# Kernel tuning notes

Hardware: AMD Instinct MI355X
Metric: run time of the kernel (lower is better)

## Reference

```python
import jax, jax.numpy as jnp
import numpy as np

NUM_NODES = 512
NUM_EDGES = 512
EMB_DIM = 128
HIDDEN = 256
NUM_INC = 8192


def setup_inputs() -> dict:
    key = jax.random.key(0)
    ks = jax.random.split(key, 8)
    X = jax.random.normal(ks[0], (NUM_NODES, EMB_DIM), dtype=jnp.float32)
    V = jax.random.randint(ks[1], (NUM_INC,), 0, NUM_NODES, dtype=jnp.int64)
    E = jax.random.randint(ks[2], (NUM_INC,), 0, NUM_EDGES, dtype=jnp.int64)
    # MLP params, torch nn.Linear layout: W (out, in), y = x @ W.T + b
    lim1 = 1.0 / np.sqrt(2 * EMB_DIM)
    W1 = jax.random.uniform(ks[3], (HIDDEN, 2 * EMB_DIM), minval=-lim1, maxval=lim1, dtype=jnp.float32)
    b1 = jax.random.uniform(ks[4], (HIDDEN,), minval=-lim1, maxval=lim1, dtype=jnp.float32)
    lim2 = 1.0 / np.sqrt(HIDDEN)
    W2 = jax.random.uniform(ks[5], (1, HIDDEN), minval=-lim2, maxval=lim2, dtype=jnp.float32)
    b2 = jax.random.uniform(ks[6], (1,), minval=-lim2, maxval=lim2, dtype=jnp.float32)
    return {"X": X, "V": V, "E": E, "W1": W1, "b1": b1, "W2": W2, "b2": b2}


def reference(X, V, E, W1, b1, W2, b2):
    d = X.shape[-1]
    # scatter-mean of gathered node embeddings into edges; empty edges -> 0 (nan_to_num)
    sums = jax.ops.segment_sum(X[V], E, num_segments=NUM_EDGES)          # (M, d)
    cnt = jax.ops.segment_sum(jnp.ones((V.shape[0],), X.dtype), E, num_segments=NUM_EDGES)
    eX = jnp.where(cnt[:, None] > 0, sums / jnp.maximum(cnt[:, None], 1.0), 0.0)
    # cat([X_expanded, eX_expanded]) @ W1.T == X @ W1[:, :d].T + eX @ W1[:, d:].T (broadcast add)
    hX = X @ W1[:, :d].T                                                 # (N, H)
    hE = eX @ W1[:, d:].T                                                # (M, H)
    hidden = jax.nn.relu(hX[:, None, :] + hE[None, :, :] + b1)           # (N, M, H)
    logits = jnp.einsum('nmh,h->nm', hidden, W2[0]) + b2[0]              # (N, M)
    prob = jax.nn.sigmoid(logits)
    prob = jnp.nan_to_num(prob, nan=0.5)
    prob = jnp.clip(prob, 1e-6, 1.0 - 1e-6)
    return prob
```

## Files before the change

### kernel.cpp

```cpp
#include <hip/hip_runtime.h>
#include <math.h>

#define NN 512
#define MM 512
#define DD 128
#define HH 256

typedef float     v4f __attribute__((ext_vector_type(4)));
typedef _Float16  h8  __attribute__((ext_vector_type(8)));
typedef _Float16  h2  __attribute__((ext_vector_type(2)));


__global__ __launch_bounds__(256) void k_stage(
    const float* __restrict__ X, const int* __restrict__ V,
    const int* __restrict__ E, const float* __restrict__ W1,
    const float* __restrict__ b1, _Float16* __restrict__ A,
    _Float16* __restrict__ C, int ninc)
{
    __shared__ int   lst[8192];
    __shared__ float eXp[2 * DD];
    __shared__ float eXs[DD];
    __shared__ int   cnt_s;

    const int b = blockIdx.x;
    const int t = threadIdx.x;

    if (b < MM) {
        if (t == 0) cnt_s = 0;
        __syncthreads();
        const int nq = ninc >> 2;
        for (int c = t; c < nq; c += 256) {
            int4 e4 = ((const int4*)E)[c];
            int base = c * 4;
            if (e4.x == b) lst[atomicAdd(&cnt_s, 1)] = V[base + 0];
            if (e4.y == b) lst[atomicAdd(&cnt_s, 1)] = V[base + 1];
            if (e4.z == b) lst[atomicAdd(&cnt_s, 1)] = V[base + 2];
            if (e4.w == b) lst[atomicAdd(&cnt_s, 1)] = V[base + 3];
        }
        __syncthreads();
        const int cnt = cnt_s;

        const int d = t & 127, half = t >> 7;
        float a0 = 0.f, a1 = 0.f;
        int j = half;
        for (; j + 2 < cnt; j += 4) {
            int v0 = lst[j], v1 = lst[j + 2];
            a0 += X[v0 * DD + d];
            a1 += X[v1 * DD + d];
        }
        for (; j < cnt; j += 2) a0 += X[lst[j] * DD + d];
        eXp[half * DD + d] = a0 + a1;
        __syncthreads();
        if (t < DD) {
            float inv = cnt > 0 ? 1.0f / (float)cnt : 0.0f;
            eXs[t] = (eXp[t] + eXp[DD + t]) * inv;
        }
        __syncthreads();

        const float* w = W1 + t * (2 * DD) + DD;
        v4f dv = (v4f)(0.f);
        #pragma unroll 8
        for (int k = 0; k < DD; k += 4)
            dv += (*(const v4f*)(w + k)) * (*(const v4f*)(eXs + k));
        C[b * HH + t] = (_Float16)(b1[t] + dv.x + dv.y + dv.z + dv.w);
    } else {
        const int r0 = (b - MM) * 4;
        const float* w  = W1 + t * (2 * DD);
        const float* x0 = X + (r0 + 0) * DD;
        const float* x1 = X + (r0 + 1) * DD;
        const float* x2 = X + (r0 + 2) * DD;
        const float* x3 = X + (r0 + 3) * DD;
        v4f acc0 = (v4f)(0.f), acc1 = (v4f)(0.f), acc2 = (v4f)(0.f), acc3 = (v4f)(0.f);
        #pragma unroll 4
        for (int k = 0; k < DD; k += 4) {
            v4f wv = *(const v4f*)(w + k);
            acc0 += wv * (*(const v4f*)(x0 + k));
            acc1 += wv * (*(const v4f*)(x1 + k));
            acc2 += wv * (*(const v4f*)(x2 + k));
            acc3 += wv * (*(const v4f*)(x3 + k));
        }
        A[(r0 + 0) * HH + t] = (_Float16)(acc0.x + acc0.y + acc0.z + acc0.w);
        A[(r0 + 1) * HH + t] = (_Float16)(acc1.x + acc1.y + acc1.z + acc1.w);
        A[(r0 + 2) * HH + t] = (_Float16)(acc2.x + acc2.y + acc2.z + acc2.w);
        A[(r0 + 3) * HH + t] = (_Float16)(acc3.x + acc3.y + acc3.z + acc3.w);
    }
}

#define ROWH 264
#define CT   (16 * ROWH)
#define WT   (32 * ROWH)

__device__ inline float dot8(h8 w, h8 a, h8 c, float acc) {
    h8 s = a + c;
    s = __builtin_elementwise_max(s, (h8)(_Float16)0.f);
    union { h8 v; h2 p[4]; } su, wu;
    su.v = s; wu.v = w;
    acc = __builtin_amdgcn_fdot2(su.p[0], wu.p[0], acc, false);
    acc = __builtin_amdgcn_fdot2(su.p[1], wu.p[1], acc, false);
    acc = __builtin_amdgcn_fdot2(su.p[2], wu.p[2], acc, false);
    acc = __builtin_amdgcn_fdot2(su.p[3], wu.p[3], acc, false);
    return acc;
}

__global__ __launch_bounds__(256) void k_pairs(
    const _Float16* __restrict__ A, const _Float16* __restrict__ C,
    const float* __restrict__ W2, const float* __restrict__ b2,
    float* __restrict__ out)
{
    __shared__ _Float16 lds[WT + 256];
    const int t  = threadIdx.x;
    const int bx = blockIdx.x;
    const int tn0 = (bx >> 5) * 16;
    const int tm0 = (bx & 31) * 16;

    lds[WT + t] = (_Float16)W2[t];
    #pragma unroll
    for (int p = 0; p < 4; ++p) {
        int g = p * 256 + t;
        int row = g >> 5, c8 = (g & 31) * 8;
        const _Float16* src;
        int dst;
        if (row < 16) { src = A + (tn0 + row) * HH + c8;        dst = row * ROWH + c8; }
        else          { src = C + (tm0 + row - 16) * HH + c8;   dst = CT + (row - 16) * ROWH + c8; }
        *(h8*)&lds[dst] = *(const h8*)src;
    }
    __syncthreads();

    const int w = t >> 6, lane = t & 63;
    const int ra = 2 * (lane & 7);
    const int rc = 2 * (lane >> 3);
    const _Float16* la = lds + ra * ROWH + w * 64;
    const _Float16* lc = lds + CT + rc * ROWH + w * 64;
    const _Float16* lw = lds + WT + w * 64;

    float a00 = 0.f, a01 = 0.f, a10 = 0.f, a11 = 0.f;
    #pragma unroll
    for (int hh = 0; hh < 64; hh += 8) {
        h8 wv  = *(const h8*)(lw + hh);
        h8 av0 = *(const h8*)(la + hh);
        h8 av1 = *(const h8*)(la + ROWH + hh);
        h8 cv0 = *(const h8*)(lc + hh);
        h8 cv1 = *(const h8*)(lc + ROWH + hh);
        a00 = dot8(wv, av0, cv0, a00);
        a01 = dot8(wv, av0, cv1, a01);
        a10 = dot8(wv, av1, cv0, a10);
        a11 = dot8(wv, av1, cv1, a11);
    }

    __syncthreads();
    float* red = (float*)lds;
    red[w * 256 + (ra + 0) * 16 + (rc + 0)] = a00;
    red[w * 256 + (ra + 0) * 16 + (rc + 1)] = a01;
    red[w * 256 + (ra + 1) * 16 + (rc + 0)] = a10;
    red[w * 256 + (ra + 1) * 16 + (rc + 1)] = a11;
    __syncthreads();

    const int p = t;
    float s = red[p] + red[256 + p] + red[512 + p] + red[768 + p] + b2[0];
    float prob = 1.0f / (1.0f + __expf(-s));
    prob = fminf(fmaxf(prob, 1e-6f), 1.0f - 1e-6f);
    out[(tn0 + (p >> 4)) * MM + tm0 + (p & 15)] = prob;
}

extern "C" void kernel_launch(void* const* d_in, const int* in_sizes, int n_in,
                              void* d_out, int out_size, void* d_ws, size_t ws_size,
                              hipStream_t stream)
{
    const float* X  = (const float*)d_in[0];
    const int*   V  = (const int*)d_in[1];
    const int*   E  = (const int*)d_in[2];
    const float* W1 = (const float*)d_in[3];
    const float* b1 = (const float*)d_in[4];
    const float* W2 = (const float*)d_in[5];
    const float* b2 = (const float*)d_in[6];

    _Float16* A = (_Float16*)d_ws;
    _Float16* C = A + NN * HH;
    float* out  = (float*)d_out;
    int ninc    = in_sizes[1];

    k_stage<<<MM + NN / 4, 256, 0, stream>>>(X, V, E, W1, b1, A, C, ninc);
    k_pairs<<<(NN / 16) * (MM / 16), 256, 0, stream>>>(A, C, W2, b2, out);
}
```

Baseline: 85.11 us.

## Batch four edges per stage block and enlarge pair tiles to 32x32

```diff
diff --git a/kernel.cpp b/kernel.cpp
--- a/kernel.cpp
+++ b/kernel.cpp
@@ -17,78 +17,112 @@
     const float* __restrict__ b1, _Float16* __restrict__ A,
     _Float16* __restrict__ C, int ninc)
 {
-    __shared__ int   lst[8192];
-    __shared__ float eXp[2 * DD];
-    __shared__ float eXs[DD];
-    __shared__ int   cnt_s;
+    __shared__ union {
+        int    lst[8192];
+        float4 w1t[64][32];
+    } u;
+    __shared__ float xr[4][128];
+    __shared__ float red[16][64];
+    __shared__ int   cnt4[4], pos4[4], off4[4];
 
     const int b = blockIdx.x;
     const int t = threadIdx.x;
-
-    if (b < MM) {
-        if (t == 0) cnt_s = 0;
+    const int w = t >> 6, lane = t & 63;
+    const bool edge = (b < 128);
+
+    if (edge) {
+        const int e0 = b * 4;
+        if (t < 4) { cnt4[t] = 0; pos4[t] = 0; }
         __syncthreads();
         const int nq = ninc >> 2;
         for (int c = t; c < nq; c += 256) {
             int4 e4 = ((const int4*)E)[c];
-            int base = c * 4;
-            if (e4.x == b) lst[atomicAdd(&cnt_s, 1)] = V[base + 0];
-            if (e4.y == b) lst[atomicAdd(&cnt_s, 1)] = V[base + 1];
-            if (e4.z == b) lst[atomicAdd(&cnt_s, 1)] = V[base + 2];
-            if (e4.w == b) lst[atomicAdd(&cnt_s, 1)] = V[base + 3];
-        }
-        __syncthreads();
-        const int cnt = cnt_s;
-
-        const int d = t & 127, half = t >> 7;
-        float a0 = 0.f, a1 = 0.f;
-        int j = half;
-        for (; j + 2 < cnt; j += 4) {
-            int v0 = lst[j], v1 = lst[j + 2];
-            a0 += X[v0 * DD + d];
-            a1 += X[v1 * DD + d];
-        }
-        for (; j < cnt; j += 2) a0 += X[lst[j] * DD + d];
-        eXp[half * DD + d] = a0 + a1;
-        __syncthreads();
-        if (t < DD) {
-            float inv = cnt > 0 ? 1.0f / (float)cnt : 0.0f;
-            eXs[t] = (eXp[t] + eXp[DD + t]) * inv;
-        }
-        __syncthreads();
-
-        const float* w = W1 + t * (2 * DD) + DD;
-        v4f dv = (v4f)(0.f);
-        #pragma unroll 8
-        for (int k = 0; k < DD; k += 4)
-            dv += (*(const v4f*)(w + k)) * (*(const v4f*)(eXs + k));
-        C[b * HH + t] = (_Float16)(b1[t] + dv.x + dv.y + dv.z + dv.w);
+            if ((unsigned)(e4.x - e0) < 4u) atomicAdd(&cnt4[e4.x - e0], 1);
+            if ((unsigned)(e4.y - e0) < 4u) atomicAdd(&cnt4[e4.y - e0], 1);
+            if ((unsigned)(e4.z - e0) < 4u) atomicAdd(&cnt4[e4.z - e0], 1);
+            if ((unsigned)(e4.w - e0) < 4u) atomicAdd(&cnt4[e4.w - e0], 1);
+        }
+        __syncthreads();
+        if (t == 0) {
+            off4[0] = 0;
+            off4[1] = cnt4[0];
+            off4[2] = cnt4[0] + cnt4[1];
+            off4[3] = off4[2] + cnt4[2];
+        }
+        __syncthreads();
+        for (int c = t; c < nq; c += 256) {
+            int4 e4 = ((const int4*)E)[c];
+            int4 v4 = ((const int4*)V)[c];
+            if ((unsigned)(e4.x - e0) < 4u) u.lst[off4[e4.x-e0] + atomicAdd(&pos4[e4.x-e0], 1)] = v4.x;
+            if ((unsigned)(e4.y - e0) < 4u) u.lst[off4[e4.y-e0] + atomicAdd(&pos4[e4.y-e0], 1)] = v4.y;
+            if ((unsigned)(e4.z - e0) < 4u) u.lst[off4[e4.z-e0] + atomicAdd(&pos4[e4.z-e0], 1)] = v4.z;
+            if ((unsigned)(e4.w - e0) < 4u) u.lst[off4[e4.w-e0] + atomicAdd(&pos4[e4.w-e0], 1)] = v4.w;
+        }
+        __syncthreads();
+        const int cnt = cnt4[w], off = off4[w];
+        float s0a=0.f,s0b=0.f,s0c=0.f,s0d=0.f, s1a=0.f,s1b=0.f,s1c=0.f,s1d=0.f;
+        int j = 0;
+        for (; j + 4 <= cnt; j += 4) {
+            int v0 = u.lst[off+j], v1 = u.lst[off+j+1], v2 = u.lst[off+j+2], v3 = u.lst[off+j+3];
+            s0a += X[v0*DD + lane];      s1a += X[v0*DD + 64 + lane];
+            s0b += X[v1*DD + lane];      s1b += X[v1*DD + 64 + lane];
+            s0c += X[v2*DD + lane];      s1c += X[v2*DD + 64 + lane];
+            s0d += X[v3*DD + lane];      s1d += X[v3*DD + 64 + lane];
+        }
+        for (; j < cnt; ++j) {
+            int v = u.lst[off+j];
+            s0a += X[v*DD + lane];       s1a += X[v*DD + 64 + lane];
+        }
+        float inv = cnt > 0 ? 1.0f / (float)cnt : 0.0f;
+        xr[w][lane]      = (s0a+s0b+s0c+s0d) * inv;
+        xr[w][lane+64]   = (s1a+s1b+s1c+s1d) * inv;
+        __syncthreads();
     } else {
-        const int r0 = (b - MM) * 4;
-        const float* w  = W1 + t * (2 * DD);
-        const float* x0 = X + (r0 + 0) * DD;
-        const float* x1 = X + (r0 + 1) * DD;
-        const float* x2 = X + (r0 + 2) * DD;
-        const float* x3 = X + (r0 + 3) * DD;
+        const int r0 = (b - 128) * 4;
+        ((float*)xr)[t]       = X[r0*DD + t];
+        ((float*)xr)[t + 256] = X[r0*DD + 256 + t];
+        __syncthreads();
+    }
+
+    const int r0row = edge ? b*4 : (b-128)*4;
+    const int koff  = edge ? DD : 0;
+    _Float16* Out   = edge ? C : A;
+
+    #pragma unroll 1
+    for (int p = 0; p < 4; ++p) {
+        const int h0 = p * 64;
+        #pragma unroll
+        for (int q = 0; q < 8; ++q) {
+            int c  = q * 256 + t;
+            int h  = c >> 5, kq = c & 31;
+            u.w1t[h][kq ^ (h & 31)] =
+                *(const float4*)&W1[(h0 + h) * (2*DD) + koff + kq * 4];
+        }
+        __syncthreads();
         v4f acc0 = (v4f)(0.f), acc1 = (v4f)(0.f), acc2 = (v4f)(0.f), acc3 = (v4f)(0.f);
-        #pragma unroll 4
-        for (int k = 0; k < DD; k += 4) {
-            v4f wv = *(const v4f*)(w + k);
-            acc0 += wv * (*(const v4f*)(x0 + k));
-            acc1 += wv * (*(const v4f*)(x1 + k));
-            acc2 += wv * (*(const v4f*)(x2 + k));
-            acc3 += wv * (*(const v4f*)(x3 + k));
-        }
-        A[(r0 + 0) * HH + t] = (_Float16)(acc0.x + acc0.y + acc0.z + acc0.w);
-        A[(r0 + 1) * HH + t] = (_Float16)(acc1.x + acc1.y + acc1.z + acc1.w);
-        A[(r0 + 2) * HH + t] = (_Float16)(acc2.x + acc2.y + acc2.z + acc2.w);
-        A[(r0 + 3) * HH + t] = (_Float16)(acc3.x + acc3.y + acc3.z + acc3.w);
-    }
-}
-
-#define ROWH 264
-#define CT   (16 * ROWH)
-#define WT   (32 * ROWH)
+        #pragma unroll
+        for (int i = 0; i < 8; ++i) {
+            int kq = w * 8 + i;
+            v4f wv = *(const v4f*)&u.w1t[lane][kq ^ (lane & 31)];
+            acc0 += wv * (*(const v4f*)&xr[0][kq*4]);
+            acc1 += wv * (*(const v4f*)&xr[1][kq*4]);
+            acc2 += wv * (*(const v4f*)&xr[2][kq*4]);
+            acc3 += wv * (*(const v4f*)&xr[3][kq*4]);
+        }
+        red[w*4 + 0][lane] = acc0.x + acc0.y + acc0.z + acc0.w;
+        red[w*4 + 1][lane] = acc1.x + acc1.y + acc1.z + acc1.w;
+        red[w*4 + 2][lane] = acc2.x + acc2.y + acc2.z + acc2.w;
+        red[w*4 + 3][lane] = acc3.x + acc3.y + acc3.z + acc3.w;
+        __syncthreads();
+        float s = red[w][lane] + red[4 + w][lane] + red[8 + w][lane] + red[12 + w][lane];
+        if (edge) s += b1[h0 + lane];
+        Out[(r0row + w) * HH + h0 + lane] = (_Float16)s;
+        __syncthreads();
+    }
+}
+
+#define CT 8192
+#define WT 16384
 
 __device__ inline float dot8(h8 w, h8 a, h8 c, float acc) {
     h8 s = a + c;
@@ -110,56 +144,77 @@
     __shared__ _Float16 lds[WT + 256];
     const int t  = threadIdx.x;
     const int bx = blockIdx.x;
-    const int tn0 = (bx >> 5) * 16;
-    const int tm0 = (bx & 31) * 16;
+    const int tn0 = (bx >> 4) * 32;
+    const int tm0 = (bx & 15) * 32;
 
     lds[WT + t] = (_Float16)W2[t];
     #pragma unroll
-    for (int p = 0; p < 4; ++p) {
-        int g = p * 256 + t;
-        int row = g >> 5, c8 = (g & 31) * 8;
-        const _Float16* src;
-        int dst;
-        if (row < 16) { src = A + (tn0 + row) * HH + c8;        dst = row * ROWH + c8; }
-        else          { src = C + (tm0 + row - 16) * HH + c8;   dst = CT + (row - 16) * ROWH + c8; }
+    for (int q = 0; q < 8; ++q) {
+        int g   = q * 256 + t;
+        int row = g >> 5, cc = g & 31, r = row & 31;
+        int dst = (row < 32 ? 0 : CT) + r * 256 + ((cc ^ (r >> 2)) << 3);
+        const _Float16* src = (row < 32) ? A + (tn0 + r) * HH + cc * 8
+                                         : C + (tm0 + r) * HH + cc * 8;
         *(h8*)&lds[dst] = *(const h8*)src;
     }
     __syncthreads();
 
-    const int w = t >> 6, lane = t & 63;
-    const int ra = 2 * (lane & 7);
-    const int rc = 2 * (lane >> 3);
-    const _Float16* la = lds + ra * ROWH + w * 64;
-    const _Float16* lc = lds + CT + rc * ROWH + w * 64;
-    const _Float16* lw = lds + WT + w * 64;
-
-    float a00 = 0.f, a01 = 0.f, a10 = 0.f, a11 = 0.f;
+    const int w  = t >> 6, lane = t & 63;
+    const int qa = lane & 7,  ra = 4 * qa;
+    const int qc = lane >> 3, rc = 4 * qc;
+    const int h0 = w * 64;
+
+    float acc[4][4];
+    #pragma unroll
+    for (int i = 0; i < 4; ++i)
+        #pragma unroll
+        for (int j = 0; j < 4; ++j) acc[i][j] = 0.f;
+
     #pragma unroll
     for (int hh = 0; hh < 64; hh += 8) {
-        h8 wv  = *(const h8*)(lw + hh);
-        h8 av0 = *(const h8*)(la + hh);
-        h8 av1 = *(const h8*)(la + ROWH + hh);
-        h8 cv0 = *(const h8*)(lc + hh);
-        h8 cv1 = *(const h8*)(lc + ROWH + hh);
-        a00 = dot8(wv, av0, cv0, a00);
-        a01 = dot8(wv, av0, cv1, a01);
-        a10 = dot8(wv, av1, cv0, a10);
-        a11 = dot8(wv, av1, cv1, a11);
+        int h  = h0 + hh;
+        int cc = h >> 3;
+        int sa = (cc ^ qa) << 3;
+        int sc = (cc ^ qc) << 3;
+        h8 wv = *(const h8*)&lds[WT + h];
+        h8 av[4], cv[4];
+        #pragma unroll
+        for (int i = 0; i < 4; ++i) av[i] = *(const h8*)&lds[(ra + i) * 256 + sa];
+        #pragma unroll
+        for (int j = 0; j < 4; ++j) cv[j] = *(const h8*)&lds[CT + (rc + j) * 256 + sc];
+        #pragma unroll
+        for (int i = 0; i < 4; ++i)
+            #pragma unroll
+            for (int j = 0; j < 4; ++j)
+                acc[i][j] = dot8(wv, av[i], cv[j], acc[i][j]);
     }
 
     __syncthreads();
     float* red = (float*)lds;
-    red[w * 256 + (ra + 0) * 16 + (rc + 0)] = a00;
-    red[w * 256 + (ra + 0) * 16 + (rc + 1)] = a01;
-    red[w * 256 + (ra + 1) * 16 + (rc + 0)] = a10;
-    red[w * 256 + (ra + 1) * 16 + (rc + 1)] = a11;
+    #pragma unroll
+    for (int i = 0; i < 4; ++i) {
+        float4 f;
+        f.x = acc[i][0]; f.y = acc[i][1]; f.z = acc[i][2]; f.w = acc[i][3];
+        *(float4*)&red[w * 1152 + (ra + i) * 36 + rc] = f;
+    }
     __syncthreads();
 
-    const int p = t;
-    float s = red[p] + red[256 + p] + red[512 + p] + red[768 + p] + b2[0];
-    float prob = 1.0f / (1.0f + __expf(-s));
-    prob = fminf(fmaxf(prob, 1e-6f), 1.0f - 1e-6f);
-    out[(tn0 + (p >> 4)) * MM + tm0 + (p & 15)] = prob;
+    const int rr = t >> 3;
+    const int c4 = (t & 7) * 4;
+    v4f s = *(const v4f*)&red[rr * 36 + c4];
+    s += *(const v4f*)&red[1152 + rr * 36 + c4];
+    s += *(const v4f*)&red[2304 + rr * 36 + c4];
+    s += *(const v4f*)&red[3456 + rr * 36 + c4];
+    const float b2v = b2[0];
+    float4 o;
+    float* op = &o.x;
+    #pragma unroll
+    for (int k = 0; k < 4; ++k) {
+        float logit = s[k] + b2v;
+        float p = 1.0f / (1.0f + __expf(-logit));
+        op[k] = fminf(fmaxf(p, 1e-6f), 1.0f - 1e-6f);
+    }
+    *(float4*)&out[(tn0 + rr) * MM + tm0 + c4] = o;
 }
 
 extern "C" void kernel_launch(void* const* d_in, const int* in_sizes, int n_in,
@@ -179,6 +234,6 @@
     float* out  = (float*)d_out;
     int ninc    = in_sizes[1];
 
-    k_stage<<<MM + NN / 4, 256, 0, stream>>>(X, V, E, W1, b1, A, C, ninc);
-    k_pairs<<<(NN / 16) * (MM / 16), 256, 0, stream>>>(A, C, W2, b2, out);
-}
+    k_stage<<<256, 256, 0, stream>>>(X, V, E, W1, b1, A, C, ninc);
+    k_pairs<<<256, 256, 0, stream>>>(A, C, W2, b2, out);
+}
```

After: 84.66 us. Within noise of the previous version (-0.5%).
